# Kernel optimization log

Hardware: AMD Instinct MI355X
Metric: run time of the kernel (lower is better)

The kernel has to match this reference:

```python
import jax, jax.numpy as jnp
import numpy as np

D_MODEL = 1024
N_HEADS = 16
D_K = 64
D_V = 64
B = 2
S = 2048
NEG = -1e9
EPS = 1e-5  # torch nn.LayerNorm default


def setup_inputs() -> dict:
    key = jax.random.key(0)
    ks = jax.random.split(key, 8)
    inp = {
        "input_Q": jax.random.normal(ks[0], (B, S, D_MODEL), jnp.float32),
        "input_K": jax.random.normal(ks[1], (B, S, D_MODEL), jnp.float32),
        "input_V": jax.random.normal(ks[2], (B, S, D_MODEL), jnp.float32),
        "attn_mask": jax.random.randint(ks[3], (B, S, S), 0, 2).astype(bool),
        # torch nn.Linear weights are [out_features, in_features]; scale like default init
        "W_Q": jax.random.normal(ks[4], (N_HEADS * D_K, D_MODEL), jnp.float32) * (1.0 / np.sqrt(D_MODEL)),
        "W_K": jax.random.normal(ks[5], (N_HEADS * D_K, D_MODEL), jnp.float32) * (1.0 / np.sqrt(D_MODEL)),
        "W_V": jax.random.normal(ks[6], (N_HEADS * D_V, D_MODEL), jnp.float32) * (1.0 / np.sqrt(D_MODEL)),
        "W_fc": jax.random.normal(ks[7], (D_MODEL, N_HEADS * D_V), jnp.float32) * (1.0 / np.sqrt(N_HEADS * D_V)),
    }
    return inp


def _layernorm(x):
    # fresh nn.LayerNorm(d_model): weight=1, bias=0
    mu = jnp.mean(x, axis=-1, keepdims=True)
    var = jnp.mean(jnp.square(x - mu), axis=-1, keepdims=True)
    return (x - mu) * jax.lax.rsqrt(var + EPS)


def reference(input_Q, input_K, input_V, attn_mask, W_Q, W_K, W_V, W_fc):
    residual = input_Q
    # projections: x @ W.T, then split heads -> [B, H, S, d]
    def split_heads(x, d):
        return x.reshape(B, S, N_HEADS, d).transpose(0, 2, 1, 3)

    Q = split_heads(input_Q @ W_Q.T, D_K)
    K = split_heads(input_K @ W_K.T, D_K)
    V = split_heads(input_V @ W_V.T, D_V)

    scores = jnp.einsum("bhqd,bhkd->bhqk", Q, K) / np.sqrt(D_K).astype(np.float32)
    scores = jnp.where(attn_mask[:, None, :, :], NEG, scores)
    attn = jax.nn.softmax(scores, axis=-1)
    context = jnp.einsum("bhqk,bhkd->bhqd", attn, V)  # [B,H,S,Dv]
    context = context.transpose(0, 2, 1, 3).reshape(B, S, N_HEADS * D_V)
    output = context @ W_fc.T
    return _layernorm(output + residual), attn
```

## Files before the change

kernel.cpp:

```cpp
#include <hip/hip_runtime.h>

#define NB 2
#define SS 2048
#define DMODEL 1024
#define NH 16
#define DHEAD 64
#define QSCALE 0.1803368867f

typedef __bf16 bf16;
typedef bf16 bf16x8 __attribute__((ext_vector_type(8)));
typedef float f32x4 __attribute__((ext_vector_type(4)));
typedef unsigned char u8;

static __device__ __forceinline__ f32x4 mfma_16x16x32(bf16x8 a, bf16x8 b, f32x4 c) {
    return __builtin_amdgcn_mfma_f32_16x16x32_bf16(a, b, c, 0, 0, 0);
}

static __device__ __forceinline__ float fast_exp2(float x) {
#if __has_builtin(__builtin_amdgcn_exp2f)
    return __builtin_amdgcn_exp2f(x);
#else
    return __expf(x * 0.6931471805599453f);
#endif
}

static __device__ __forceinline__ bf16x8 cvt8(float4 u, float4 v) {
    bf16x8 r;
    r[0]=(bf16)u.x; r[1]=(bf16)u.y; r[2]=(bf16)u.z; r[3]=(bf16)u.w;
    r[4]=(bf16)v.x; r[5]=(bf16)v.y; r[6]=(bf16)v.z; r[7]=(bf16)v.w;
    return r;
}

__global__ __launch_bounds__(256) void pack_mask(const int* __restrict__ m,
                                                 u8* __restrict__ mb, int n4)
{
    const int i = blockIdx.x * blockDim.x + threadIdx.x;
    if (i < n4) {
        const int4 v = ((const int4*)m)[i];
        uchar4 o;
        o.x = (u8)v.x; o.y = (u8)v.y; o.z = (u8)v.z; o.w = (u8)v.w;
        ((uchar4*)mb)[i] = o;
    }
}

__global__ __launch_bounds__(256) void gemm_xwt(const float* __restrict__ A,
                                                const float* __restrict__ W,
                                                void* __restrict__ out, int mode,
                                                float scale)
{
    __shared__ bf16 As[128][40];
    __shared__ bf16 Ws[64][40];

    const int t  = threadIdx.x;
    const int wv = t >> 6, ln = t & 63, lo = ln & 15, qd = ln >> 4;
    const int m0 = blockIdx.y << 7;
    const int n0 = blockIdx.x << 6;

    const int arow = t >> 1, acol = (t & 1) << 4;
    const int wrow = t >> 2, wcol = (t & 3) << 3;
    const float* aptr = A + (size_t)(m0 + arow) * DMODEL + acol;
    const float* wptr = W + (size_t)(n0 + wrow) * DMODEL + wcol;

    f32x4 acc[2][4];
    #pragma unroll
    for (int i = 0; i < 2; ++i)
        #pragma unroll
        for (int j = 0; j < 4; ++j) acc[i][j] = (f32x4){0.f,0.f,0.f,0.f};

    float4 a0 = *(const float4*)(aptr + 0);
    float4 a1 = *(const float4*)(aptr + 4);
    float4 a2 = *(const float4*)(aptr + 8);
    float4 a3 = *(const float4*)(aptr + 12);
    float4 w0 = *(const float4*)(wptr + 0);
    float4 w1 = *(const float4*)(wptr + 4);

    for (int k0 = 0; k0 < DMODEL; k0 += 32) {
        __syncthreads();
        *(bf16x8*)&As[arow][acol]     = cvt8(a0, a1);
        *(bf16x8*)&As[arow][acol + 8] = cvt8(a2, a3);
        *(bf16x8*)&Ws[wrow][wcol]     = cvt8(w0, w1);
        if (k0 + 32 < DMODEL) {
            a0 = *(const float4*)(aptr + k0 + 32);
            a1 = *(const float4*)(aptr + k0 + 36);
            a2 = *(const float4*)(aptr + k0 + 40);
            a3 = *(const float4*)(aptr + k0 + 44);
            w0 = *(const float4*)(wptr + k0 + 32);
            w1 = *(const float4*)(wptr + k0 + 36);
        }
        __syncthreads();
        bf16x8 af0 = *(const bf16x8*)&As[(wv << 5) + lo][qd << 3];
        bf16x8 af1 = *(const bf16x8*)&As[(wv << 5) + 16 + lo][qd << 3];
        #pragma unroll
        for (int j = 0; j < 4; ++j) {
            bf16x8 bw = *(const bf16x8*)&Ws[(j << 4) + lo][qd << 3];
            acc[0][j] = mfma_16x16x32(af0, bw, acc[0][j]);
            acc[1][j] = mfma_16x16x32(af1, bw, acc[1][j]);
        }
    }

    #pragma unroll
    for (int i = 0; i < 2; ++i) {
        #pragma unroll
        for (int j = 0; j < 4; ++j) {
            #pragma unroll
            for (int r = 0; r < 4; ++r) {
                const int m = m0 + (wv << 5) + (i << 4) + (qd << 2) + r;
                const int n = n0 + (j << 4) + lo;
                const float v = acc[i][j][r] * scale;
                if (mode == 0) {
                    ((bf16*)out)[(size_t)m * DMODEL + n] = (bf16)v;
                } else if (mode == 1) {
                    ((bf16*)out)[((size_t)(m >> 11) * 1024 + n) * SS + (m & (SS - 1))] = (bf16)v;
                } else {
                    ((float*)out)[(size_t)m * DMODEL + n] = v;
                }
            }
        }
    }
}

__global__ __launch_bounds__(256) void attn_fused(const bf16* __restrict__ Qp,
                                                  const bf16* __restrict__ Kp,
                                                  const bf16* __restrict__ Vt,
                                                  const u8* __restrict__ mb,
                                                  float* __restrict__ attn_out,
                                                  float* __restrict__ ctx)
{
    __shared__ bf16 Ks[2][32][72];
    __shared__ bf16 Pb[4][16][40];

    const int t  = threadIdx.x;
    const int wv = t >> 6, ln = t & 63, lo = ln & 15, qd = ln >> 4;
    const int q0 = blockIdx.x << 6;
    const int h  = blockIdx.y, b = blockIdx.z;
    const int bh = b * NH + h;

    const bf16* qsrc = Qp + (size_t)(b * SS + q0 + (wv << 4) + lo) * DMODEL + h * DHEAD + (qd << 3);
    const bf16x8 qa0 = *(const bf16x8*)qsrc;
    const bf16x8 qa1 = *(const bf16x8*)(qsrc + 32);

    const int srow = t >> 3, scol = (t & 7) << 3;
    const bf16* kbase = Kp + (size_t)(b * SS + srow) * DMODEL + h * DHEAD + scol;

    const u8* mrp[4];
    #pragma unroll
    for (int r = 0; r < 4; ++r)
        mrp[r] = mb + ((size_t)b * SS + q0 + (wv << 4) + (qd << 2) + r) * SS;

    const bf16* vbase = Vt + ((size_t)bh * DHEAD + lo) * SS + (qd << 3);

    f32x4 o[4];
    float lr[4] = {0.f, 0.f, 0.f, 0.f};
    #pragma unroll
    for (int j = 0; j < 4; ++j) o[j] = (f32x4){0.f,0.f,0.f,0.f};

    bf16x8 kreg = *(const bf16x8*)kbase;
    *(bf16x8*)&Ks[0][srow][scol] = kreg;
    kreg = *(const bf16x8*)(kbase + (size_t)32 * DMODEL);
    __syncthreads();

    for (int c = 0; c < 64; ++c) {
        if (c < 63) {
            *(bf16x8*)&Ks[(c + 1) & 1][srow][scol] = kreg;
            if (c < 62) kreg = *(const bf16x8*)(kbase + (size_t)(c + 2) * 32 * DMODEL);
        }
        const bf16 (*kb)[72] = Ks[c & 1];
        bf16x8 k00 = *(const bf16x8*)&kb[lo][qd << 3];
        bf16x8 k01 = *(const bf16x8*)&kb[lo][32 + (qd << 3)];
        bf16x8 k10 = *(const bf16x8*)&kb[16 + lo][qd << 3];
        bf16x8 k11 = *(const bf16x8*)&kb[16 + lo][32 + (qd << 3)];
        f32x4 s0 = (f32x4){0.f,0.f,0.f,0.f};
        s0 = mfma_16x16x32(qa0, k00, s0);
        s0 = mfma_16x16x32(qa1, k01, s0);
        f32x4 s1 = (f32x4){0.f,0.f,0.f,0.f};
        s1 = mfma_16x16x32(qa0, k10, s1);
        s1 = mfma_16x16x32(qa1, k11, s1);
        const int kc0 = c << 5;
        #pragma unroll
        for (int r = 0; r < 4; ++r) {
            const float e0 = mrp[r][kc0 + lo]      ? 0.f : fast_exp2(s0[r]);
            const float e1 = mrp[r][kc0 + 16 + lo] ? 0.f : fast_exp2(s1[r]);
            lr[r] += e0 + e1;
            Pb[wv][(qd << 2) + r][lo]      = (bf16)e0;
            Pb[wv][(qd << 2) + r][16 + lo] = (bf16)e1;
        }
        bf16x8 pa = *(const bf16x8*)&Pb[wv][lo][qd << 3];
        #pragma unroll
        for (int j = 0; j < 4; ++j) {
            bf16x8 vb = *(const bf16x8*)(vbase + (size_t)(j << 4) * SS + kc0);
            o[j] = mfma_16x16x32(pa, vb, o[j]);
        }
        __syncthreads();
    }

    #pragma unroll
    for (int r = 0; r < 4; ++r) {
        #pragma unroll
        for (int d = 1; d < 16; d <<= 1) lr[r] += __shfl_xor(lr[r], d);
    }
    float Li[4];
    #pragma unroll
    for (int r = 0; r < 4; ++r) Li[r] = 1.f / lr[r];

    #pragma unroll
    for (int j = 0; j < 4; ++j) {
        #pragma unroll
        for (int r = 0; r < 4; ++r) {
            ctx[(size_t)(b * SS + q0 + (wv << 4) + (qd << 2) + r) * DMODEL
                + h * DHEAD + (j << 4) + lo] = o[j][r] * Li[r];
        }
    }

    kreg = *(const bf16x8*)kbase;
    *(bf16x8*)&Ks[0][srow][scol] = kreg;
    kreg = *(const bf16x8*)(kbase + (size_t)32 * DMODEL);
    __syncthreads();

    float* aout = attn_out + ((size_t)bh * SS + q0 + (wv << 4) + (qd << 2)) * SS;

    for (int c = 0; c < 64; ++c) {
        if (c < 63) {
            *(bf16x8*)&Ks[(c + 1) & 1][srow][scol] = kreg;
            if (c < 62) kreg = *(const bf16x8*)(kbase + (size_t)(c + 2) * 32 * DMODEL);
        }
        const bf16 (*kb)[72] = Ks[c & 1];
        bf16x8 k00 = *(const bf16x8*)&kb[lo][qd << 3];
        bf16x8 k01 = *(const bf16x8*)&kb[lo][32 + (qd << 3)];
        bf16x8 k10 = *(const bf16x8*)&kb[16 + lo][qd << 3];
        bf16x8 k11 = *(const bf16x8*)&kb[16 + lo][32 + (qd << 3)];
        f32x4 s0 = (f32x4){0.f,0.f,0.f,0.f};
        s0 = mfma_16x16x32(qa0, k00, s0);
        s0 = mfma_16x16x32(qa1, k01, s0);
        f32x4 s1 = (f32x4){0.f,0.f,0.f,0.f};
        s1 = mfma_16x16x32(qa0, k10, s1);
        s1 = mfma_16x16x32(qa1, k11, s1);
        const int kc0 = c << 5;
        #pragma unroll
        for (int r = 0; r < 4; ++r) {
            const float p0 = mrp[r][kc0 + lo]      ? 0.f : fast_exp2(s0[r]) * Li[r];
            const float p1 = mrp[r][kc0 + 16 + lo] ? 0.f : fast_exp2(s1[r]) * Li[r];
            aout[(size_t)r * SS + kc0 + lo]      = p0;
            aout[(size_t)r * SS + kc0 + 16 + lo] = p1;
        }
        __syncthreads();
    }
}

__global__ __launch_bounds__(256) void ln_resid(const float* __restrict__ O,
                                                const float* __restrict__ resid,
                                                float* __restrict__ out)
{
    const int row = blockIdx.x;
    const int t = threadIdx.x;
    const size_t base = (size_t)row * DMODEL + ((size_t)t << 2);
    const float4 o  = *(const float4*)(O + base);
    const float4 rs = *(const float4*)(resid + base);
    const float x0 = o.x + rs.x, x1 = o.y + rs.y, x2 = o.z + rs.z, x3 = o.w + rs.w;
    float s  = x0 + x1 + x2 + x3;
    float ss = x0*x0 + x1*x1 + x2*x2 + x3*x3;
    #pragma unroll
    for (int d = 32; d > 0; d >>= 1) {
        s  += __shfl_xor(s, d);
        ss += __shfl_xor(ss, d);
    }
    __shared__ float ws1[4], ws2[4];
    if ((t & 63) == 0) { ws1[t >> 6] = s; ws2[t >> 6] = ss; }
    __syncthreads();
    s  = ws1[0] + ws1[1] + ws1[2] + ws1[3];
    ss = ws2[0] + ws2[1] + ws2[2] + ws2[3];
    const float mu  = s * (1.f / DMODEL);
    const float var = ss * (1.f / DMODEL) - mu * mu;
    const float inv = rsqrtf(var + 1e-5f);
    float4 y;
    y.x = (x0 - mu) * inv; y.y = (x1 - mu) * inv;
    y.z = (x2 - mu) * inv; y.w = (x3 - mu) * inv;
    *(float4*)(out + base) = y;
}

extern "C" void kernel_launch(void* const* d_in, const int* in_sizes, int n_in,
                              void* d_out, int out_size, void* d_ws, size_t ws_size,
                              hipStream_t stream)
{
    const float* inQ = (const float*)d_in[0];
    const float* inK = (const float*)d_in[1];
    const float* inV = (const float*)d_in[2];
    const int*   msk = (const int*)d_in[3];
    const float* WQ  = (const float*)d_in[4];
    const float* WK  = (const float*)d_in[5];
    const float* WV  = (const float*)d_in[6];
    const float* Wfc = (const float*)d_in[7];

    float* out_ln   = (float*)d_out;
    float* out_attn = out_ln + (size_t)NB * SS * DMODEL;

    char* w = (char*)d_ws;
    bf16*  Qp   = (bf16*)(w);
    bf16*  Kp   = (bf16*)(w + (size_t)8  * 1024 * 1024);
    bf16*  Vt   = (bf16*)(w + (size_t)16 * 1024 * 1024);
    float* ctx  = (float*)(w + (size_t)24 * 1024 * 1024);
    u8*    mkb  = (u8*)  (w + (size_t)40 * 1024 * 1024);
    float* Obuf = (float*)(w + (size_t)40 * 1024 * 1024);

    dim3 blk(256);
    const int n4 = (NB * SS * SS) / 4;
    pack_mask<<<dim3(n4 / 256), blk, 0, stream>>>(msk, mkb, n4);

    dim3 gp(DMODEL / 64, (NB * SS) / 128);
    gemm_xwt<<<gp, blk, 0, stream>>>(inQ, WQ, (void*)Qp, 0, QSCALE);
    gemm_xwt<<<gp, blk, 0, stream>>>(inK, WK, (void*)Kp, 0, 1.0f);
    gemm_xwt<<<gp, blk, 0, stream>>>(inV, WV, (void*)Vt, 1, 1.0f);
    attn_fused<<<dim3(SS / 64, NH, NB), blk, 0, stream>>>(Qp, Kp, Vt, mkb, out_attn, ctx);
    gemm_xwt<<<gp, blk, 0, stream>>>(ctx, Wfc, (void*)Obuf, 2, 1.0f);
    ln_resid<<<NB * SS, blk, 0, stream>>>(Obuf, inQ, out_ln);
}
```

Measured before the change: 977.9 us.

## Pre-convert GEMM operands to bf16, use 128x128 tiles, swizzle block order

Adds a conversion kernel that turns the fp32 activations and weights into bf16 before each projection GEMM. The GEMM now reads bf16 operands and uses 128x128 output tiles with a 2x2 warp layout. Both the GEMM and the attention kernel get a 1D grid with a swizzled block order to improve L2 locality. The attention kernel writes its context output in bf16, which halves that traffic. In exchange it adds extra conversion launches and extra fp32-to-bf16 memory passes, and the larger tiles mean only 256 GEMM blocks.

After: 966.5 us. Within noise of the previous version (-1.2%).

```diff
diff --git a/kernel.cpp b/kernel.cpp
--- a/kernel.cpp
+++ b/kernel.cpp
@@ -43,69 +43,89 @@
     }
 }
 
-__global__ __launch_bounds__(256) void gemm_xwt(const float* __restrict__ A,
-                                                const float* __restrict__ W,
-                                                void* __restrict__ out, int mode,
-                                                float scale)
+__global__ __launch_bounds__(256) void cvt_pair(const float* __restrict__ s0, bf16* __restrict__ d0, int n0_8,
+                                                const float* __restrict__ s1, bf16* __restrict__ d1, int n1_8)
+{
+    const int i = blockIdx.x * blockDim.x + threadIdx.x;
+    if (i < n0_8) {
+        float4 u = ((const float4*)s0)[(size_t)i * 2];
+        float4 v = ((const float4*)s0)[(size_t)i * 2 + 1];
+        ((bf16x8*)d0)[i] = cvt8(u, v);
+    } else if (i < n0_8 + n1_8) {
+        const int j = i - n0_8;
+        float4 u = ((const float4*)s1)[(size_t)j * 2];
+        float4 v = ((const float4*)s1)[(size_t)j * 2 + 1];
+        ((bf16x8*)d1)[j] = cvt8(u, v);
+    }
+}
+
+__global__ __launch_bounds__(256) void gemm_bt(const bf16* __restrict__ A,
+                                               const bf16* __restrict__ W,
+                                               void* __restrict__ out, int mode,
+                                               float scale)
 {
     __shared__ bf16 As[128][40];
-    __shared__ bf16 Ws[64][40];
+    __shared__ bf16 Ws[128][40];
 
     const int t  = threadIdx.x;
     const int wv = t >> 6, ln = t & 63, lo = ln & 15, qd = ln >> 4;
-    const int m0 = blockIdx.y << 7;
-    const int n0 = blockIdx.x << 6;
-
-    const int arow = t >> 1, acol = (t & 1) << 4;
-    const int wrow = t >> 2, wcol = (t & 3) << 3;
-    const float* aptr = A + (size_t)(m0 + arow) * DMODEL + acol;
-    const float* wptr = W + (size_t)(n0 + wrow) * DMODEL + wcol;
-
-    f32x4 acc[2][4];
-    #pragma unroll
-    for (int i = 0; i < 2; ++i)
+    const int wm = wv >> 1, wn = wv & 1;
+
+    const int flat = blockIdx.x;
+    const int swz  = ((flat & 7) << 5) + (flat >> 3);
+    const int m0   = (swz >> 3) << 7;
+    const int n0   = (swz & 7) << 7;
+
+    const int srow = t >> 2, scol = (t & 3) << 3;
+    const bf16* ap = A + (size_t)(m0 + srow) * DMODEL + scol;
+    const bf16* wp = W + (size_t)(n0 + srow) * DMODEL + scol;
+
+    f32x4 acc[4][4];
+    #pragma unroll
+    for (int i = 0; i < 4; ++i)
         #pragma unroll
         for (int j = 0; j < 4; ++j) acc[i][j] = (f32x4){0.f,0.f,0.f,0.f};
 
-    float4 a0 = *(const float4*)(aptr + 0);
-    float4 a1 = *(const float4*)(aptr + 4);
-    float4 a2 = *(const float4*)(aptr + 8);
-    float4 a3 = *(const float4*)(aptr + 12);
-    float4 w0 = *(const float4*)(wptr + 0);
-    float4 w1 = *(const float4*)(wptr + 4);
+    bf16x8 a0 = *(const bf16x8*)ap;
+    bf16x8 a1 = *(const bf16x8*)(ap + (size_t)64 * DMODEL);
+    bf16x8 w0 = *(const bf16x8*)wp;
+    bf16x8 w1 = *(const bf16x8*)(wp + (size_t)64 * DMODEL);
 
     for (int k0 = 0; k0 < DMODEL; k0 += 32) {
         __syncthreads();
-        *(bf16x8*)&As[arow][acol]     = cvt8(a0, a1);
-        *(bf16x8*)&As[arow][acol + 8] = cvt8(a2, a3);
-        *(bf16x8*)&Ws[wrow][wcol]     = cvt8(w0, w1);
+        *(bf16x8*)&As[srow][scol]      = a0;
+        *(bf16x8*)&As[64 + srow][scol] = a1;
+        *(bf16x8*)&Ws[srow][scol]      = w0;
+        *(bf16x8*)&Ws[64 + srow][scol] = w1;
         if (k0 + 32 < DMODEL) {
-            a0 = *(const float4*)(aptr + k0 + 32);
-            a1 = *(const float4*)(aptr + k0 + 36);
-            a2 = *(const float4*)(aptr + k0 + 40);
-            a3 = *(const float4*)(aptr + k0 + 44);
-            w0 = *(const float4*)(wptr + k0 + 32);
-            w1 = *(const float4*)(wptr + k0 + 36);
+            a0 = *(const bf16x8*)(ap + k0 + 32);
+            a1 = *(const bf16x8*)(ap + (size_t)64 * DMODEL + k0 + 32);
+            w0 = *(const bf16x8*)(wp + k0 + 32);
+            w1 = *(const bf16x8*)(wp + (size_t)64 * DMODEL + k0 + 32);
         }
         __syncthreads();
-        bf16x8 af0 = *(const bf16x8*)&As[(wv << 5) + lo][qd << 3];
-        bf16x8 af1 = *(const bf16x8*)&As[(wv << 5) + 16 + lo][qd << 3];
-        #pragma unroll
-        for (int j = 0; j < 4; ++j) {
-            bf16x8 bw = *(const bf16x8*)&Ws[(j << 4) + lo][qd << 3];
-            acc[0][j] = mfma_16x16x32(af0, bw, acc[0][j]);
-            acc[1][j] = mfma_16x16x32(af1, bw, acc[1][j]);
-        }
-    }
-
-    #pragma unroll
-    for (int i = 0; i < 2; ++i) {
+        bf16x8 af[4], wf[4];
+        #pragma unroll
+        for (int i = 0; i < 4; ++i)
+            af[i] = *(const bf16x8*)&As[(wm << 6) + (i << 4) + lo][qd << 3];
+        #pragma unroll
+        for (int j = 0; j < 4; ++j)
+            wf[j] = *(const bf16x8*)&Ws[(wn << 6) + (j << 4) + lo][qd << 3];
+        #pragma unroll
+        for (int i = 0; i < 4; ++i)
+            #pragma unroll
+            for (int j = 0; j < 4; ++j)
+                acc[i][j] = mfma_16x16x32(af[i], wf[j], acc[i][j]);
+    }
+
+    #pragma unroll
+    for (int i = 0; i < 4; ++i) {
         #pragma unroll
         for (int j = 0; j < 4; ++j) {
             #pragma unroll
             for (int r = 0; r < 4; ++r) {
-                const int m = m0 + (wv << 5) + (i << 4) + (qd << 2) + r;
-                const int n = n0 + (j << 4) + lo;
+                const int m = m0 + (wm << 6) + (i << 4) + (qd << 2) + r;
+                const int n = n0 + (wn << 6) + (j << 4) + lo;
                 const float v = acc[i][j][r] * scale;
                 if (mode == 0) {
                     ((bf16*)out)[(size_t)m * DMODEL + n] = (bf16)v;
@@ -124,15 +144,19 @@
                                                   const bf16* __restrict__ Vt,
                                                   const u8* __restrict__ mb,
                                                   float* __restrict__ attn_out,
-                                                  float* __restrict__ ctx)
+                                                  bf16* __restrict__ ctxb)
 {
     __shared__ bf16 Ks[2][32][72];
     __shared__ bf16 Pb[4][16][40];
 
     const int t  = threadIdx.x;
     const int wv = t >> 6, ln = t & 63, lo = ln & 15, qd = ln >> 4;
-    const int q0 = blockIdx.x << 6;
-    const int h  = blockIdx.y, b = blockIdx.z;
+
+    const int flat = blockIdx.x;
+    const int swz  = ((flat & 7) << 7) + (flat >> 3);
+    const int q0 = (swz & 31) << 6;
+    const int h  = (swz >> 5) & 15;
+    const int b  = swz >> 9;
     const int bh = b * NH + h;
 
     const bf16* qsrc = Qp + (size_t)(b * SS + q0 + (wv << 4) + lo) * DMODEL + h * DHEAD + (qd << 3);
@@ -206,8 +230,8 @@
     for (int j = 0; j < 4; ++j) {
         #pragma unroll
         for (int r = 0; r < 4; ++r) {
-            ctx[(size_t)(b * SS + q0 + (wv << 4) + (qd << 2) + r) * DMODEL
-                + h * DHEAD + (j << 4) + lo] = o[j][r] * Li[r];
+            ctxb[(size_t)(b * SS + q0 + (wv << 4) + (qd << 2) + r) * DMODEL
+                 + h * DHEAD + (j << 4) + lo] = (bf16)(o[j][r] * Li[r]);
         }
     }
 
@@ -294,22 +318,39 @@
     float* out_attn = out_ln + (size_t)NB * SS * DMODEL;
 
     char* w = (char*)d_ws;
+    const size_t MB = 1024 * 1024;
     bf16*  Qp   = (bf16*)(w);
-    bf16*  Kp   = (bf16*)(w + (size_t)8  * 1024 * 1024);
-    bf16*  Vt   = (bf16*)(w + (size_t)16 * 1024 * 1024);
-    float* ctx  = (float*)(w + (size_t)24 * 1024 * 1024);
-    u8*    mkb  = (u8*)  (w + (size_t)40 * 1024 * 1024);
-    float* Obuf = (float*)(w + (size_t)40 * 1024 * 1024);
+    bf16*  Kp   = (bf16*)(w + 8  * MB);
+    bf16*  Vt   = (bf16*)(w + 16 * MB);
+    bf16*  ctxb = (bf16*)(w + 24 * MB);
+    bf16*  Abf  = (bf16*)(w + 32 * MB);
+    u8*    mkb  = (u8*)  (w + 40 * MB);
+    bf16*  Wbf  = (bf16*)(w + 48 * MB);
+    float* Obuf = (float*)(w + 32 * MB);
 
     dim3 blk(256);
+
     const int n4 = (NB * SS * SS) / 4;
     pack_mask<<<dim3(n4 / 256), blk, 0, stream>>>(msk, mkb, n4);
 
-    dim3 gp(DMODEL / 64, (NB * SS) / 128);
-    gemm_xwt<<<gp, blk, 0, stream>>>(inQ, WQ, (void*)Qp, 0, QSCALE);
-    gemm_xwt<<<gp, blk, 0, stream>>>(inK, WK, (void*)Kp, 0, 1.0f);
-    gemm_xwt<<<gp, blk, 0, stream>>>(inV, WV, (void*)Vt, 1, 1.0f);
-    attn_fused<<<dim3(SS / 64, NH, NB), blk, 0, stream>>>(Qp, Kp, Vt, mkb, out_attn, ctx);
-    gemm_xwt<<<gp, blk, 0, stream>>>(ctx, Wfc, (void*)Obuf, 2, 1.0f);
-    ln_resid<<<NB * SS, blk, 0, stream>>>(Obuf, inQ, out_ln);
-}
+    const int nIn8 = (NB * SS * DMODEL) / 8;
+    const int nW8  = (DMODEL * DMODEL) / 8;
+    const int cvtBoth = (nIn8 + nW8 + 255) / 256;
+    const int cvtW    = (nW8 + 255) / 256;
+
+    cvt_pair<<<dim3(cvtBoth), blk, 0, stream>>>(inQ, Abf, nIn8, WQ, Wbf, nW8);
+    gemm_bt<<<dim3(256), blk, 0, stream>>>(Abf, Wbf, (void*)Qp, 0, QSCALE);
+
+    cvt_pair<<<dim3(cvtBoth), blk, 0, stream>>>(inK, Abf, nIn8, WK, Wbf, nW8);
+    gemm_bt<<<dim3(256), blk, 0, stream>>>(Abf, Wbf, (void*)Kp, 0, 1.0f);
+
+    cvt_pair<<<dim3(cvtBoth), blk, 0, stream>>>(inV, Abf, nIn8, WV, Wbf, nW8);
+    gemm_bt<<<dim3(256), blk, 0, stream>>>(Abf, Wbf, (void*)Vt, 1, 1.0f);
+
+    attn_fused<<<dim3(SS / 64 * NH * NB), blk, 0, stream>>>(Qp, Kp, Vt, mkb, out_attn, ctxb);
+
+    cvt_pair<<<dim3(cvtW), blk, 0, stream>>>(Wfc, Wbf, nW8, (const float*)0, (bf16*)0, 0);
+    gemm_bt<<<dim3(256), blk, 0, stream>>>(ctxb, Wbf, (void*)Obuf, 2, 1.0f);
+
+    ln_resid<<<dim3(NB * SS), blk, 0, stream>>>(Obuf, inQ, out_ln);
+}
```
